# Kernel tuning notes

Measured on AMD Instinct MI355X. Metric: run time of the kernel, lower is better.

## Reference

```python
import jax, jax.numpy as jnp
import numpy as np

N, E, DIN, HID, G, L = 50000, 200000, 128, 128, 64, 6
H1, H2 = 8, 4
EPS_LN, EPS_BN = 1e-5, 1e-5


def setup_inputs() -> dict:
    key = jax.random.key(0)
    ks = iter(jax.random.split(key, 32))
    def nrm(shape, scale=0.05):
        return jax.random.normal(next(ks), shape, dtype=jnp.float32) * scale
    z = lambda *s: jnp.zeros(s, jnp.float32)
    o = lambda *s: jnp.ones(s, jnp.float32)
    return {
        'x': jax.random.normal(next(ks), (N, DIN), dtype=jnp.float32),
        'edge_index': jax.random.randint(next(ks), (2, E), 0, N),
        'batch': jnp.sort(jax.random.randint(next(ks), (N,), 0, G)),
        'W1': nrm((DIN, H1 * HID)), 'a_src1': nrm((H1, HID)), 'a_dst1': nrm((H1, HID)), 'b1': z(H1 * HID),
        'W2': nrm((H1 * HID, H2 * HID)), 'a_src2': nrm((H2, HID)), 'a_dst2': nrm((H2, HID)), 'b2': z(H2 * HID),
        'W3': nrm((H2 * HID, HID)), 'b3': z(HID),
        'wq': nrm((L, HID, HID)), 'bq': z(L, HID), 'wk': nrm((L, HID, HID)), 'bk': z(L, HID),
        'wv': nrm((L, HID, HID)), 'bv': z(L, HID), 'wo': nrm((L, HID, HID)), 'bo': z(L, HID),
        'ln1g': o(L, HID), 'ln1b': z(L, HID), 'ln2g': o(L, HID), 'ln2b': z(L, HID),
        'wf1': nrm((L, HID, 4 * HID)), 'bf1': z(L, 4 * HID), 'wf2': nrm((L, 4 * HID, HID)), 'bf2': z(L, HID),
        'bn1_g': o(2 * HID), 'bn1_b': z(2 * HID),
        'fc1_w': nrm((2 * HID, HID // 2)), 'fc1_b': z(HID // 2),
        'bn2_g': o(HID // 2), 'bn2_b': z(HID // 2),
        'fc2_w': nrm((HID // 2, 2)), 'fc2_b': z(2),
    }


def _ln(x, g, b):
    mu = x.mean(-1, keepdims=True)
    v = ((x - mu) ** 2).mean(-1, keepdims=True)
    return (x - mu) * jax.lax.rsqrt(v + EPS_LN) * g + b


def _gat(x, src, dst, W, a_s, a_d, b, heads):
    # PyG GATConv: message src -> dst, segment softmax over incoming edges per dst.
    h = (x @ W).reshape(x.shape[0], heads, -1)           # [N, H, C]
    e = jax.nn.leaky_relu((h * a_s).sum(-1)[src] + (h * a_d).sum(-1)[dst], 0.2)  # [E, H]
    m = jax.ops.segment_max(e, dst, num_segments=N)
    ex = jnp.exp(e - jnp.where(jnp.isfinite(m), m, 0.0)[dst])
    s = jax.ops.segment_sum(ex, dst, num_segments=N)
    alpha = ex / (s[dst] + 1e-16)
    out = jax.ops.segment_sum(alpha[:, :, None] * h[src], dst, num_segments=N)
    return out.reshape(N, -1) + b


def _forward(x, edge_index, batch, W1, a_src1, a_dst1, b1, W2, a_src2, a_dst2, b2, W3, b3,
             wq, bq, wk, bk, wv, bv, wo, bo, ln1g, ln1b, ln2g, ln2b, wf1, bf1, wf2, bf2,
             bn1_g, bn1_b, fc1_w, fc1_b, bn2_g, bn2_b, fc2_w, fc2_b):
    loop = jnp.arange(N, dtype=edge_index.dtype)
    src = jnp.concatenate([edge_index[0], loop])          # add self-loops (PyG default)
    dst = jnp.concatenate([edge_index[1], loop])
    h = jax.nn.elu(_gat(x, src, dst, W1, a_src1, a_dst1, b1, H1))
    h = jax.nn.elu(_gat(h, src, dst, W2, a_src2, a_dst2, b2, H2))
    # GCNConv with symmetric normalization (self-loops already included)
    deg = jax.ops.segment_sum(jnp.ones(src.shape, h.dtype), dst, num_segments=N)
    dinv = jnp.where(deg > 0, jax.lax.rsqrt(jnp.maximum(deg, 1e-12)), 0.0)
    norm = dinv[src] * dinv[dst]
    h = jax.nn.elu(jax.ops.segment_sum(norm[:, None] * (h @ W3)[src], dst, num_segments=N) + b3)
    # TransformerEncoder over seq_len=1 (h3.unsqueeze(1)): softmax over one key == 1,
    # so MHA output == Wo @ (Wv h + bv) + bo exactly; q/k have no effect on the output.
    for l in range(L):
        sa = (h @ wv[l] + bv[l]) @ wo[l] + bo[l]
        h = _ln(h + sa, ln1g[l], ln1b[l])
        ff = jax.nn.gelu(h @ wf1[l] + bf1[l], approximate=False) @ wf2[l] + bf2[l]
        h = _ln(h + ff, ln2g[l], ln2b[l])
    # global mean / max pool over graphs
    cnt = jax.ops.segment_sum(jnp.ones((N,), h.dtype), batch, num_segments=G)
    hm = jax.ops.segment_sum(h, batch, num_segments=G) / jnp.maximum(cnt, 1.0)[:, None]
    hx = jax.ops.segment_max(h, batch, num_segments=G)
    hx = jnp.where(jnp.isfinite(hx), hx, 0.0)
    hc = jnp.concatenate([hm, hx], axis=1)                # [G, 2*HID]
    bn_s = 1.0 / np.sqrt(1.0 + EPS_BN)                    # eval BN: running stats (0, 1)
    hc = hc * bn_s * bn1_g + bn1_b
    hc = jax.nn.elu(hc @ fc1_w + fc1_b)
    hc = hc * bn_s * bn2_g + bn2_b
    return hc @ fc2_w + fc2_b                             # [G, 2]


def reference(x, edge_index, batch, W1, a_src1, a_dst1, b1, W2, a_src2, a_dst2, b2, W3, b3,
              wq, bq, wk, bk, wv, bv, wo, bo, ln1g, ln1b, ln2g, ln2b, wf1, bf1, wf2, bf2,
              bn1_g, bn1_b, fc1_w, fc1_b, bn2_g, bn2_b, fc2_w, fc2_b):
    return _forward(x, edge_index, batch, W1, a_src1, a_dst1, b1, W2, a_src2, a_dst2, b2, W3, b3,
                    wq, bq, wk, bk, wv, bv, wo, bo, ln1g, ln1b, ln2g, ln2b, wf1, bf1, wf2, bf2,
                    bn1_g, bn1_b, fc1_w, fc1_b, bn2_g, bn2_b, fc2_w, fc2_b)
```

## Files before the change

kernel.cpp:

```cpp
#include <hip/hip_runtime.h>
#include <hip/hip_bf16.h>
#include <math.h>

#define NN 50000
#define EE 200000
#define ET 250000
#define GG 64
#define LL 6

using short8 = __attribute__((ext_vector_type(8))) short;
using f32x4  = __attribute__((ext_vector_type(4))) float;
typedef unsigned short ushortT;

__device__ __forceinline__ float elu1(float x) { return x > 0.f ? x : expm1f(x); }
__device__ __forceinline__ float gelu_exact(float x) {
    return 0.5f * x * (1.f + erff(x * 0.70710678118654752440f));
}
__device__ __forceinline__ short f2bf(float f) {
    __hip_bfloat16 h = __float2bfloat16(f);
    return *reinterpret_cast<short*>(&h);
}
__device__ __forceinline__ float bf2f(ushortT u) {
    return __uint_as_float(((unsigned)u) << 16);
}
__device__ __forceinline__ void accum8(float* acc, float a, uint4 d) {
    acc[0] += a * bf2f((ushortT)(d.x & 0xffff));
    acc[1] += a * bf2f((ushortT)(d.x >> 16));
    acc[2] += a * bf2f((ushortT)(d.y & 0xffff));
    acc[3] += a * bf2f((ushortT)(d.y >> 16));
    acc[4] += a * bf2f((ushortT)(d.z & 0xffff));
    acc[5] += a * bf2f((ushortT)(d.z >> 16));
    acc[6] += a * bf2f((ushortT)(d.w & 0xffff));
    acc[7] += a * bf2f((ushortT)(d.w >> 16));
}

__global__ void count_deg_kernel(const int* __restrict__ ei, int* __restrict__ deg) {
    int e = blockIdx.x * 256 + threadIdx.x;
    if (e >= ET) return;
    int dst = (e < EE) ? ei[EE + e] : (e - EE);
    atomicAdd(&deg[dst], 1);
}

__global__ void scan_kernel(const int* __restrict__ deg, int* __restrict__ row_ptr, int n) {
    __shared__ int s[1024];
    int tid = threadIdx.x;
    const int per = (n + 1023) / 1024;
    int lo = tid * per, hi = min(lo + per, n);
    int sum = 0;
    for (int i = lo; i < hi; i++) sum += deg[i];
    s[tid] = sum;
    __syncthreads();
    for (int off = 1; off < 1024; off <<= 1) {
        int t = (tid >= off) ? s[tid - off] : 0;
        __syncthreads();
        s[tid] += t;
        __syncthreads();
    }
    int run = s[tid] - sum;
    for (int i = lo; i < hi; i++) { row_ptr[i] = run; run += deg[i]; }
    if (tid == 1023) row_ptr[n] = s[1023];
}

__global__ void fill_csr_kernel(const int* __restrict__ ei, const int* __restrict__ row_ptr,
                                int* __restrict__ cursor, int* __restrict__ edge_src) {
    int e = blockIdx.x * 256 + threadIdx.x;
    if (e >= ET) return;
    int src, dst;
    if (e < EE) { src = ei[e]; dst = ei[EE + e]; }
    else        { src = e - EE; dst = e - EE; }
    int pos = atomicAdd(&cursor[dst], 1);
    edge_src[row_ptr[dst] + pos] = src;
}

__global__ void dinv_kernel(const int* __restrict__ row_ptr, float* __restrict__ dinv) {
    int n = blockIdx.x * 256 + threadIdx.x;
    if (n >= NN) return;
    int d = row_ptr[n + 1] - row_ptr[n];
    dinv[n] = (d > 0) ? rsqrtf((float)d) : 0.f;
}

__global__ void wvwo_kernel(const float* __restrict__ wv, const float* __restrict__ wo,
                            const float* __restrict__ bv, const float* __restrict__ bo,
                            float* __restrict__ Wvo, float* __restrict__ bvo) {
    int l = blockIdx.y;
    const float* Wv = wv + l * 16384;
    const float* Wo = wo + l * 16384;
    int tid = blockIdx.x * 256 + threadIdx.x;
    if (tid < 16384) {
        int r = tid >> 7, c = tid & 127;
        float s = 0.f;
        for (int k = 0; k < 128; k++) s += Wv[r * 128 + k] * Wo[k * 128 + c];
        Wvo[l * 16384 + tid] = s;
    }
    if (blockIdx.x == 0 && threadIdx.x < 128) {
        int c = threadIdx.x;
        float s = bo[l * 128 + c];
        for (int k = 0; k < 128; k++) s += bv[l * 128 + k] * Wo[k * 128 + c];
        bvo[l * 128 + c] = s;
    }
}

__global__ void bprep_kernel(const float* __restrict__ B, short* __restrict__ Bp,
                             int K, int N, int ldb, long srcStride) {
    int layer = blockIdx.y;
    const float* Bsrc = B + srcStride * layer;
    short* Bd = Bp + (size_t)K * N * layer;
    int total = (K >> 5) * (N >> 4) * 64;
    int tid = blockIdx.x * 256 + threadIdx.x;
    if (tid >= total) return;
    int l = tid & 63;
    int rest = tid >> 6;
    int kbc = K >> 5;
    int kb = rest % kbc;
    int c16 = rest / kbc;
    int n = c16 * 16 + (l & 15);
    int kbase = kb * 32 + (l >> 4) * 8;
    short v[8];
#pragma unroll
    for (int j = 0; j < 8; j++) v[j] = f2bf(Bsrc[(size_t)(kbase + j) * ldb + n]);
    *(uint4*)(Bd + (size_t)tid * 8) = *(uint4*)v;
}

__global__ void cast_bf16_kernel(const float* __restrict__ in, short* __restrict__ out, int n4) {
    int i = blockIdx.x * 256 + threadIdx.x;
    if (i >= n4) return;
    float4 v = *(const float4*)(in + (size_t)i * 4);
    short s[4] = { f2bf(v.x), f2bf(v.y), f2bf(v.z), f2bf(v.w) };
    *(uint2*)(out + (size_t)i * 4) = *(uint2*)s;
}

template <int EPI, bool BIAS, bool OUTBF16, int NSPLIT, int KBC,
          bool TMAJ = false, bool ATILE32 = false>
__global__ __launch_bounds__(256) void gemm_bf16_kernel(
    const short* __restrict__ A, const short* __restrict__ Bp,
    const float* __restrict__ bias, void* __restrict__ Cv,
    const float* __restrict__ a_s, const float* __restrict__ a_d,
    float* __restrict__ as_out, float* __restrict__ ad_out, int asH,
    const ushortT* __restrict__ Rres, const float* __restrict__ lng,
    const float* __restrict__ lnb, float* __restrict__ Qout,
    __hip_bfloat16* __restrict__ Qbout,
    int M, int K, int Nc) {
    __shared__ short Bs[(KBC > 0) ? KBC * 4096 : 8192];
    int t = threadIdx.x;
    int w = t >> 6, l = t & 63;
    int ln = l & 15, lq = l >> 4;
    int MBceil = (M + 63) >> 6;
    int bx = blockIdx.x;
    int xcd = bx & 7, idx = bx >> 3;
    int t2 = idx % NSPLIT;
    int mb = (idx / NSPLIT) * 8 + xcd;
    if (mb >= MBceil) return;
    int bm = mb * 64 + w * 16;
    int arow = bm + ln;
    bool aok = arow < M;
    int rowb = bm + lq * 4;
    const short* Ap = A + (size_t)arow * K + lq * 8;

    auto aload = [&](int kb) -> short8 {
        if (!aok) return (short8){0, 0, 0, 0, 0, 0, 0, 0};
        const short* p;
        if constexpr (ATILE32)
            p = A + ((size_t)kb * M + arow) * 32 + lq * 8;
        else
            p = Ap + kb * 32;
        return *(const short8*)p;
    };

    f32x4 acc[8];
#pragma unroll
    for (int j = 0; j < 8; j++) acc[j] = (f32x4){0.f, 0.f, 0.f, 0.f};

    if constexpr (KBC > 0) {
        {
            const uint4* src = (const uint4*)(Bp + (size_t)t2 * KBC * 4096);
            uint4* dst = (uint4*)Bs;
#pragma unroll
            for (int i = 0; i < KBC * 2; i++)
                dst[i * 256 + t] = src[i * 256 + t];
        }
        short8 af[KBC];
#pragma unroll
        for (int kb = 0; kb < KBC; kb++)
            af[kb] = aload(kb);
        __syncthreads();
#pragma unroll
        for (int kb = 0; kb < KBC; kb++)
#pragma unroll
            for (int ct = 0; ct < 8; ct++) {
                short8 bfr = *(const short8*)(Bs + ((ct * KBC + kb) * 64 + l) * 8);
                acc[ct] = __builtin_amdgcn_mfma_f32_16x16x32_bf16(af[kb], bfr, acc[ct], 0, 0, 0);
            }
    } else {
        int kbc = K >> 5;
        int sct = t >> 5, spart = t & 31;
        auto stage = [&](int buf, int kb) {
            const uint4* src = (const uint4*)(Bp + ((size_t)(t2 * 8 + sct) * kbc + kb) * 512);
            uint4* dst = (uint4*)(Bs + buf * 4096 + sct * 512);
            dst[spart * 2]     = src[spart * 2];
            dst[spart * 2 + 1] = src[spart * 2 + 1];
        };
        stage(0, 0);
        __syncthreads();
        for (int kb = 0; kb < kbc; kb++) {
            if (kb + 1 < kbc) stage((kb + 1) & 1, kb + 1);
            short8 af = aload(kb);
            const short* bsb = Bs + (kb & 1) * 4096;
#pragma unroll
            for (int ct = 0; ct < 8; ct++) {
                short8 bfr = *(const short8*)(bsb + (ct * 64 + l) * 8);
                acc[ct] = __builtin_amdgcn_mfma_f32_16x16x32_bf16(af, bfr, acc[ct], 0, 0, 0);
            }
            __syncthreads();
        }
    }

    if (EPI == 2) {
        const float* asv = a_s + t2 * 128;
        const float* adv = a_d + t2 * 128;
#pragma unroll
        for (int reg = 0; reg < 4; reg++) {
            float vs = 0.f, vd = 0.f;
#pragma unroll
            for (int ct = 0; ct < 8; ct++) {
                int colL = ct * 16 + ln;
                float av = acc[ct][reg];
                vs += av * asv[colL];
                vd += av * adv[colL];
            }
            vs += __shfl_xor(vs, 1); vs += __shfl_xor(vs, 2);
            vs += __shfl_xor(vs, 4); vs += __shfl_xor(vs, 8);
            vd += __shfl_xor(vd, 1); vd += __shfl_xor(vd, 2);
            vd += __shfl_xor(vd, 4); vd += __shfl_xor(vd, 8);
            int row = rowb + reg;
            if (ln == 0 && row < M) {
                as_out[(size_t)row * asH + t2] = vs;
                ad_out[(size_t)row * asH + t2] = vd;
            }
        }
    }
    if (EPI == 3) {
        float v[8][4];
#pragma unroll
        for (int ct = 0; ct < 8; ct++) {
            int col = ct * 16 + ln;
            float bv_ = bias[col];
#pragma unroll
            for (int reg = 0; reg < 4; reg++) {
                int row = rowb + reg;
                float r = (row < M) ? bf2f(Rres[(size_t)row * 128 + col]) : 0.f;
                v[ct][reg] = acc[ct][reg] + bv_ + r;
            }
        }
#pragma unroll
        for (int reg = 0; reg < 4; reg++) {
            float s = 0.f;
#pragma unroll
            for (int ct = 0; ct < 8; ct++) s += v[ct][reg];
            s += __shfl_xor(s, 1); s += __shfl_xor(s, 2);
            s += __shfl_xor(s, 4); s += __shfl_xor(s, 8);
            float mean = s * (1.f / 128.f);
            float s2 = 0.f;
#pragma unroll
            for (int ct = 0; ct < 8; ct++) { float d = v[ct][reg] - mean; s2 += d * d; }
            s2 += __shfl_xor(s2, 1); s2 += __shfl_xor(s2, 2);
            s2 += __shfl_xor(s2, 4); s2 += __shfl_xor(s2, 8);
            float rstd = rsqrtf(s2 * (1.f / 128.f) + 1e-5f);
            int row = rowb + reg;
            if (row < M) {
#pragma unroll
                for (int ct = 0; ct < 8; ct++) {
                    int col = ct * 16 + ln;
                    float o = (v[ct][reg] - mean) * rstd * lng[col] + lnb[col];
                    Qbout[(size_t)row * 128 + col] = __float2bfloat16(o);
                    if (Qout) Qout[(size_t)row * 128 + col] = o;
                }
            }
        }
    }
    if (EPI == 0 || EPI == 1 || EPI == 2) {
#pragma unroll
        for (int ct = 0; ct < 8; ct++) {
            int col = t2 * 128 + ct * 16 + ln;
            float bv_ = BIAS ? bias[col] : 0.f;
#pragma unroll
            for (int reg = 0; reg < 4; reg++) {
                int row = rowb + reg;
                if (row < M) {
                    float v = acc[ct][reg] + bv_;
                    if (EPI == 1) v = gelu_exact(v);
                    if (OUTBF16) {
                        size_t addr;
                        if constexpr (TMAJ)
                            addr = ((size_t)(col >> 5) * M + row) * 32 + (col & 31);
                        else
                            addr = (size_t)row * Nc + col;
                        ((__hip_bfloat16*)Cv)[addr] = __float2bfloat16(v);
                    } else {
                        ((float*)Cv)[(size_t)row * Nc + col] = v;
                    }
                }
            }
        }
    }
}

template <int H>
__global__ __launch_bounds__(256) void gat_alpha_kernel(
    const float* __restrict__ as_, const float* __restrict__ ad_,
    const int* __restrict__ row_ptr, const int* __restrict__ edge_src,
    float* __restrict__ exA, float* __restrict__ exS, int n_nodes) {
    const int GS = 64 / H;
    int node = blockIdx.x * 4 + (threadIdx.x >> 6);
    if (node >= n_nodes) return;
    int l = threadIdx.x & 63;
    int h = l / GS;
    int lig = l % GS;
    int start = row_ptr[node];
    int deg = row_ptr[node + 1] - start;
    float adn = ad_[(size_t)node * H + h];
    float m = -1e30f;
    for (int j = lig; j < deg; j += GS) {
        int s = edge_src[start + j];
        float e = as_[(size_t)s * H + h] + adn;
        e = e > 0.f ? e : 0.2f * e;
        m = fmaxf(m, e);
    }
#pragma unroll
    for (int mask = 1; mask < GS; mask <<= 1)
        m = fmaxf(m, __shfl_xor(m, mask));
    float S = 0.f;
    for (int j = lig; j < deg; j += GS) {
        int s = edge_src[start + j];
        float e = as_[(size_t)s * H + h] + adn;
        e = e > 0.f ? e : 0.2f * e;
        float ex = expf(e - m);
        exA[(size_t)h * ET + (start + j)] = ex;
        S += ex;
    }
#pragma unroll
    for (int mask = 1; mask < GS; mask <<= 1)
        S += __shfl_xor(S, mask);
    if (lig == 0) exS[(size_t)h * n_nodes + node] = S;
}

__global__ __launch_bounds__(256) void gat_agg_tiled_kernel(
    const ushortT* __restrict__ hT, const float* __restrict__ exA,
    const float* __restrict__ exS, const float* __restrict__ bias,
    const int* __restrict__ row_ptr, const int* __restrict__ edge_src,
    __hip_bfloat16* __restrict__ outT, int n_nodes, int NB) {
    int bx = blockIdx.x;
    int xcd = bx & 7, rest = bx >> 3;
    int tl = rest / NB, nb = rest - tl * NB;
    int tile = tl * 8 + xcd;
    int nl = threadIdx.x >> 2, q = threadIdx.x & 3;
    int node = nb * 64 + nl;
    if (node >= n_nodes) return;
    int hb = tile >> 2;
    const ushortT* __restrict__ base = hT + (size_t)tile * n_nodes * 32 + q * 8;
    const float* __restrict__ exAh = exA + (size_t)hb * ET;
    int start = row_ptr[node];
    int deg = row_ptr[node + 1] - start;
    float acc[8];
#pragma unroll
    for (int c = 0; c < 8; c++) acc[c] = 0.f;
    for (int j = 0; j < deg; j++) {
        int s = edge_src[start + j];
        float a = exAh[start + j];
        uint4 d = *(const uint4*)(base + (size_t)s * 32);
        accum8(acc, a, d);
    }
    float inv = 1.f / (exS[(size_t)hb * n_nodes + node] + 1e-16f);
    const float* bp = bias + tile * 32 + q * 8;
    short o[8];
#pragma unroll
    for (int c = 0; c < 8; c++)
        o[c] = f2bf(elu1(acc[c] * inv + bp[c]));
    *(uint4*)(outT + ((size_t)tile * n_nodes + node) * 32 + q * 8) = *(uint4*)o;
}

__global__ __launch_bounds__(256, 2) void gcn_agg_kernel(
    const ushortT* __restrict__ hp, const float* __restrict__ dinv,
    const float* __restrict__ b3, const int* __restrict__ row_ptr,
    const int* __restrict__ edge_src,
    __hip_bfloat16* __restrict__ outb, int n_nodes) {
    int node = blockIdx.x * 2 + (threadIdx.x >> 7);
    int c = threadIdx.x & 127;
    if (node >= n_nodes) return;
    int start = row_ptr[node];
    int deg = row_ptr[node + 1] - start;
    float dn = dinv[node];
    float acc = 0.f;
    auto LS = [&](int j) { return edge_src[start + min(j, deg - 1)]; };
    int s0 = LS(0), s1 = LS(1), s2 = LS(2), s3 = LS(3);
    int s4 = LS(4), s5 = LS(5), s6 = LS(6), s7 = LS(7);
    auto HW = [&](int s, int j, float& h, float& w) {
        h = bf2f(hp[(size_t)s * 128 + c]);
        w = (j < deg) ? dinv[s] * dn : 0.f;
    };
    float h0, h1, h2, h3, h4, h5, h6, h7;
    float w0, w1, w2, w3, w4, w5, w6, w7;
    HW(s0, 0, h0, w0); HW(s1, 1, h1, w1); HW(s2, 2, h2, w2); HW(s3, 3, h3, w3);
    HW(s4, 4, h4, w4); HW(s5, 5, h5, w5); HW(s6, 6, h6, w6); HW(s7, 7, h7, w7);
    int j0 = 0;
    while (true) {
        int jn = j0 + 8;
        bool more = jn < deg;
        float g0, g1, g2, g3, g4, g5, g6, g7;
        float v0 = 0.f, v1 = 0.f, v2 = 0.f, v3 = 0.f;
        float v4 = 0.f, v5 = 0.f, v6 = 0.f, v7 = 0.f;
        if (more) {
            int t0 = LS(jn),     t1 = LS(jn + 1), t2 = LS(jn + 2), t3 = LS(jn + 3);
            int t4 = LS(jn + 4), t5 = LS(jn + 5), t6 = LS(jn + 6), t7 = LS(jn + 7);
            HW(t0, jn,     g0, v0); HW(t1, jn + 1, g1, v1);
            HW(t2, jn + 2, g2, v2); HW(t3, jn + 3, g3, v3);
            HW(t4, jn + 4, g4, v4); HW(t5, jn + 5, g5, v5);
            HW(t6, jn + 6, g6, v6); HW(t7, jn + 7, g7, v7);
        }
        acc += w0 * h0 + w1 * h1 + w2 * h2 + w3 * h3
             + w4 * h4 + w5 * h5 + w6 * h6 + w7 * h7;
        if (!more) break;
        h0 = g0; h1 = g1; h2 = g2; h3 = g3;
        h4 = g4; h5 = g5; h6 = g6; h7 = g7;
        w0 = v0; w1 = v1; w2 = v2; w3 = v3;
        w4 = v4; w5 = v5; w6 = v6; w7 = v7;
        j0 = jn;
    }
    outb[(size_t)node * 128 + c] = __float2bfloat16(elu1(acc + b3[c]));
}

__global__ void pool1_kernel(const float* __restrict__ Q, const int* __restrict__ batch,
                             float* __restrict__ psum, float* __restrict__ pmax, int n_nodes) {
    int g = blockIdx.x, seg = blockIdx.y;
    int c = threadIdx.x;
    int lo, hi;
    {
        int l = 0, h = n_nodes;
        while (l < h) { int mid = (l + h) >> 1; if (batch[mid] < g) l = mid + 1; else h = mid; }
        lo = l;
        l = lo; h = n_nodes;
        while (l < h) { int mid = (l + h) >> 1; if (batch[mid] < g + 1) l = mid + 1; else h = mid; }
        hi = l;
    }
    int len = hi - lo;
    int a = lo + (int)((long)len * seg / 8);
    int b = lo + (int)((long)len * (seg + 1) / 8);
    float s = 0.f, mx = -INFINITY;
    for (int n = a; n < b; n++) {
        float v = Q[(size_t)n * 128 + c];
        s += v;
        mx = fmaxf(mx, v);
    }
    psum[(g * 8 + seg) * 128 + c] = s;
    pmax[(g * 8 + seg) * 128 + c] = mx;
}

__global__ void pool2_kernel(const float* __restrict__ psum, const float* __restrict__ pmax,
                             const int* __restrict__ batch,
                             const float* __restrict__ bn1g, const float* __restrict__ bn1b,
                             float* __restrict__ hc, int n_nodes) {
    int g = blockIdx.x;
    int c = threadIdx.x;
    int lo, hi;
    {
        int l = 0, h = n_nodes;
        while (l < h) { int mid = (l + h) >> 1; if (batch[mid] < g) l = mid + 1; else h = mid; }
        lo = l;
        l = lo; h = n_nodes;
        while (l < h) { int mid = (l + h) >> 1; if (batch[mid] < g + 1) l = mid + 1; else h = mid; }
        hi = l;
    }
    int cnt = hi - lo;
    float s = 0.f, mx = -INFINITY;
    for (int seg = 0; seg < 8; seg++) {
        s += psum[(g * 8 + seg) * 128 + c];
        mx = fmaxf(mx, pmax[(g * 8 + seg) * 128 + c]);
    }
    float hm = s / fmaxf((float)cnt, 1.f);
    float hx = (cnt > 0 && isfinite(mx)) ? mx : 0.f;
    const float bn_s = 0.99999500003749968f;
    hc[g * 256 + c]       = hm * bn_s * bn1g[c] + bn1b[c];
    hc[g * 256 + 128 + c] = hx * bn_s * bn1g[128 + c] + bn1b[128 + c];
}

__global__ void head_kernel(const float* __restrict__ hc,
                            const float* __restrict__ fc1w, const float* __restrict__ fc1b,
                            const float* __restrict__ bn2g, const float* __restrict__ bn2b,
                            const float* __restrict__ fc2w, const float* __restrict__ fc2b,
                            float* __restrict__ out) {
    int g = blockIdx.x;
    int j = threadIdx.x;
    const float bn_s = 0.99999500003749968f;
    float acc = fc1b[j];
    for (int i = 0; i < 256; i++) acc += hc[g * 256 + i] * fc1w[i * 64 + j];
    acc = elu1(acc);
    acc = acc * bn_s * bn2g[j] + bn2b[j];
    __shared__ float sv[64];
    sv[j] = acc;
    __syncthreads();
    if (j < 2) {
        float o = fc2b[j];
        for (int i = 0; i < 64; i++) o += sv[i] * fc2w[i * 2 + j];
        out[g * 2 + j] = o;
    }
}

extern "C" void kernel_launch(void* const* d_in, const int* in_sizes, int n_in,
                              void* d_out, int out_size, void* d_ws, size_t ws_size,
                              hipStream_t stream) {
    const float* x    = (const float*)d_in[0];
    const int*   ei   = (const int*)d_in[1];
    const int*   batch= (const int*)d_in[2];
    const float* W1   = (const float*)d_in[3];
    const float* as1  = (const float*)d_in[4];
    const float* ad1  = (const float*)d_in[5];
    const float* b1   = (const float*)d_in[6];
    const float* W2   = (const float*)d_in[7];
    const float* as2  = (const float*)d_in[8];
    const float* ad2  = (const float*)d_in[9];
    const float* b2   = (const float*)d_in[10];
    const float* W3   = (const float*)d_in[11];
    const float* b3   = (const float*)d_in[12];
    const float* wv   = (const float*)d_in[17];
    const float* bv   = (const float*)d_in[18];
    const float* wo   = (const float*)d_in[19];
    const float* bo   = (const float*)d_in[20];
    const float* ln1g = (const float*)d_in[21];
    const float* ln1b = (const float*)d_in[22];
    const float* ln2g = (const float*)d_in[23];
    const float* ln2b = (const float*)d_in[24];
    const float* wf1  = (const float*)d_in[25];
    const float* bf1  = (const float*)d_in[26];
    const float* wf2  = (const float*)d_in[27];
    const float* bf2  = (const float*)d_in[28];
    const float* bn1g = (const float*)d_in[29];
    const float* bn1b = (const float*)d_in[30];
    const float* fc1w = (const float*)d_in[31];
    const float* fc1b = (const float*)d_in[32];
    const float* bn2g = (const float*)d_in[33];
    const float* bn2b = (const float*)d_in[34];
    const float* fc2w = (const float*)d_in[35];
    const float* fc2b = (const float*)d_in[36];
    float* out = (float*)d_out;

    char* wsb = (char*)d_ws;
    short* xb    = (short*)wsb;
    float* exAf  = (float*)wsb;
    float* exSf  = (float*)(wsb + 8000000);
    short* h1t   = (short*)(wsb + 12800000);
    short* h2t   = (short*)(wsb + 12800000);
    short* h3pre = (short*)(wsb + 12800000);
    short* FFb   = (short*)(wsb + 25600000);
    short* bh1   = (short*)(wsb + 115200000);
    short* bh2   = (short*)(wsb + 115200000);
    float* fQ    = (float*)(wsb + 128000000);
    short* Qb    = (short*)(wsb + 153600000);
    char* tail = wsb + 217600000;
    short* W1p  = (short*)tail;  tail += 262144;
    short* W2p  = (short*)tail;  tail += 1048576;
    short* W3p  = (short*)tail;  tail += 131072;
    short* Wvop = (short*)tail;  tail += 196608;
    short* wf1p = (short*)tail;  tail += 786432;
    short* wf2p = (short*)tail;  tail += 786432;
    float* Wvo  = (float*)tail;  tail += 393216;
    float* bvo  = (float*)tail;  tail += 3072;
    float* fAS  = (float*)tail;  tail += 1600000;
    float* fAD  = (float*)tail;  tail += 1600000;
    float* fDv  = (float*)tail;  tail += 200000;
    float* psum = (float*)tail;  tail += 262144;
    float* pmax = (float*)tail;  tail += 262144;
    float* fHC  = (float*)tail;  tail += 65536;
    int* iDeg   = (int*)tail;    tail += 200000;
    int* iRP    = (int*)tail;    tail += 200004;
    int* iCur   = (int*)tail;    tail += 200000;
    int* iES    = (int*)tail;    tail += 1000000;

    hipMemsetAsync(iDeg, 0, NN * sizeof(int), stream);
    hipMemsetAsync(iCur, 0, NN * sizeof(int), stream);

    count_deg_kernel<<<(ET + 255) / 256, 256, 0, stream>>>(ei, iDeg);
    scan_kernel<<<1, 1024, 0, stream>>>(iDeg, iRP, NN);
    fill_csr_kernel<<<(ET + 255) / 256, 256, 0, stream>>>(ei, iRP, iCur, iES);
    dinv_kernel<<<(NN + 255) / 256, 256, 0, stream>>>(iRP, fDv);

    wvwo_kernel<<<dim3(64, 6), 256, 0, stream>>>(wv, wo, bv, bo, Wvo, bvo);
    auto bprep = [&](const float* B, short* Bp, int K, int N, int ldb, long sStride, int layers) {
        int total = (K >> 5) * (N >> 4) * 64;
        dim3 grid((total + 255) / 256, layers);
        bprep_kernel<<<grid, 256, 0, stream>>>(B, Bp, K, N, ldb, sStride);
    };
    bprep(W1, W1p, 128, 1024, 1024, 0, 1);
    bprep(W2, W2p, 1024, 512, 512, 0, 1);
    bprep(W3, W3p, 512, 128, 128, 0, 1);
    bprep(Wvo, Wvop, 128, 128, 128, 16384, 6);
    bprep(wf1, wf1p, 128, 512, 512, 65536, 6);
    bprep(wf2, wf2p, 512, 128, 128, 65536, 6);
    cast_bf16_kernel<<<(NN * 128 / 4 + 255) / 256, 256, 0, stream>>>(x, xb, NN * 128 / 4);

    const int MB64 = (NN + 63) / 64;
    const int MBp = ((MB64 + 7) / 8) * 8;
    const int NB = (NN + 63) / 64;

    gemm_bf16_kernel<2, false, true, 8, 4, true, false><<<MBp * 8, 256, 0, stream>>>(
        xb, W1p, nullptr, h1t, as1, ad1, fAS, fAD, 8,
        nullptr, nullptr, nullptr, nullptr, nullptr, NN, 128, 1024);
    gat_alpha_kernel<8><<<(NN + 3) / 4, 256, 0, stream>>>(
        fAS, fAD, iRP, iES, exAf, exSf, NN);
    gat_agg_tiled_kernel<<<4 * NB * 8, 256, 0, stream>>>(
        (const ushortT*)h1t, exAf, exSf, b1, iRP, iES, (__hip_bfloat16*)bh1, NN, NB);
    gemm_bf16_kernel<2, false, true, 4, 0, true, true><<<MBp * 4, 256, 0, stream>>>(
        bh1, W2p, nullptr, h2t, as2, ad2, fAS, fAD, 4,
        nullptr, nullptr, nullptr, nullptr, nullptr, NN, 1024, 512);
    gat_alpha_kernel<4><<<(NN + 3) / 4, 256, 0, stream>>>(
        fAS, fAD, iRP, iES, exAf, exSf, NN);
    gat_agg_tiled_kernel<<<2 * NB * 8, 256, 0, stream>>>(
        (const ushortT*)h2t, exAf, exSf, b2, iRP, iES, (__hip_bfloat16*)bh2, NN, NB);
    gemm_bf16_kernel<0, false, true, 1, 0, false, true><<<MBp, 256, 0, stream>>>(
        bh2, W3p, nullptr, h3pre, nullptr, nullptr, nullptr, nullptr, 0,
        nullptr, nullptr, nullptr, nullptr, nullptr, NN, 512, 128);
    gcn_agg_kernel<<<(NN + 1) / 2, 256, 0, stream>>>(
        (const ushortT*)h3pre, fDv, b3, iRP, iES, (__hip_bfloat16*)Qb, NN);
    for (int l = 0; l < LL; l++) {
        gemm_bf16_kernel<3, true, false, 1, 4><<<MBp, 256, 0, stream>>>(
            Qb, Wvop + l * 16384, bvo + l * 128, nullptr, nullptr, nullptr, nullptr, nullptr, 0,
            (const ushortT*)Qb, ln1g + l * 128, ln1b + l * 128, nullptr, (__hip_bfloat16*)Qb,
            NN, 128, 128);
        gemm_bf16_kernel<1, true, true, 4, 4><<<MBp * 4, 256, 0, stream>>>(
            Qb, wf1p + l * 65536, bf1 + l * 512, FFb, nullptr, nullptr, nullptr, nullptr, 0,
            nullptr, nullptr, nullptr, nullptr, nullptr, NN, 128, 512);
        gemm_bf16_kernel<3, true, false, 1, 0><<<MBp, 256, 0, stream>>>(
            FFb, wf2p + l * 65536, bf2 + l * 128, nullptr, nullptr, nullptr, nullptr, nullptr, 0,
            (const ushortT*)Qb, ln2g + l * 128, ln2b + l * 128,
            (l == LL - 1) ? fQ : nullptr, (__hip_bfloat16*)Qb, NN, 512, 128);
    }
    pool1_kernel<<<dim3(GG, 8), 128, 0, stream>>>(fQ, batch, psum, pmax, NN);
    pool2_kernel<<<GG, 128, 0, stream>>>(psum, pmax, batch, bn1g, bn1b, fHC, NN);
    head_kernel<<<GG, 64, 0, stream>>>(fHC, fc1w, fc1b, bn2g, bn2b, fc2w, fc2b, out);
}
```

Measured before the change: 1.308 ms.

## Sort nodes by degree before GAT aggregation to balance wavefront work

Adds a counting sort of nodes by in-degree (histogram, 64-bucket scan, scatter) that builds a permutation. The GAT aggregation kernels then process nodes in permuted order, so lanes in a wavefront have similar edge-loop trip counts and diverge less. The cost is three small extra kernels plus an indirect node lookup. Output writes and exS reads become scattered, which loses the coalescing of the original node order.

Result: slower. 1.768 ms (+35.2%).

```diff
diff --git a/kernel.cpp b/kernel.cpp
--- a/kernel.cpp
+++ b/kernel.cpp
@@ -77,6 +77,33 @@
     if (n >= NN) return;
     int d = row_ptr[n + 1] - row_ptr[n];
     dinv[n] = (d > 0) ? rsqrtf((float)d) : 0.f;
+}
+
+__global__ void hist_deg_kernel(const int* __restrict__ row_ptr, int* __restrict__ hist) {
+    int n = blockIdx.x * 256 + threadIdx.x;
+    if (n >= NN) return;
+    int d = min(row_ptr[n + 1] - row_ptr[n], 63);
+    atomicAdd(&hist[d], 1);
+}
+__global__ void scan64_kernel(int* __restrict__ hist) {
+    __shared__ int s[64];
+    int t = threadIdx.x;
+    s[t] = hist[t];
+    __syncthreads();
+    if (t == 0) {
+        int run = 0;
+        for (int i = 0; i < 64; i++) { int v = s[i]; s[i] = run; run += v; }
+    }
+    __syncthreads();
+    hist[t] = s[t];
+}
+__global__ void scatter_perm_kernel(const int* __restrict__ row_ptr,
+                                    int* __restrict__ hist, int* __restrict__ perm) {
+    int n = blockIdx.x * 256 + threadIdx.x;
+    if (n >= NN) return;
+    int d = min(row_ptr[n + 1] - row_ptr[n], 63);
+    int p = atomicAdd(&hist[d], 1);
+    perm[p] = n;
 }
 
 __global__ void wvwo_kernel(const float* __restrict__ wv, const float* __restrict__ wo,
@@ -347,14 +374,16 @@
     const ushortT* __restrict__ hT, const float* __restrict__ exA,
     const float* __restrict__ exS, const float* __restrict__ bias,
     const int* __restrict__ row_ptr, const int* __restrict__ edge_src,
+    const int* __restrict__ perm,
     __hip_bfloat16* __restrict__ outT, int n_nodes, int NB) {
     int bx = blockIdx.x;
     int xcd = bx & 7, rest = bx >> 3;
     int tl = rest / NB, nb = rest - tl * NB;
     int tile = tl * 8 + xcd;
     int nl = threadIdx.x >> 2, q = threadIdx.x & 3;
-    int node = nb * 64 + nl;
-    if (node >= n_nodes) return;
+    int idx = nb * 64 + nl;
+    if (idx >= n_nodes) return;
+    int node = perm[idx];
     int hb = tile >> 2;
     const ushortT* __restrict__ base = hT + (size_t)tile * n_nodes * 32 + q * 8;
     const float* __restrict__ exAh = exA + (size_t)hb * ET;
@@ -581,6 +610,11 @@
     scan_kernel<<<1, 1024, 0, stream>>>(iDeg, iRP, NN);
     fill_csr_kernel<<<(ET + 255) / 256, 256, 0, stream>>>(ei, iRP, iCur, iES);
     dinv_kernel<<<(NN + 255) / 256, 256, 0, stream>>>(iRP, fDv);
+    int* perm = iCur;
+    hipMemsetAsync(iDeg, 0, 64 * sizeof(int), stream);
+    hist_deg_kernel<<<(NN + 255) / 256, 256, 0, stream>>>(iRP, iDeg);
+    scan64_kernel<<<1, 64, 0, stream>>>(iDeg);
+    scatter_perm_kernel<<<(NN + 255) / 256, 256, 0, stream>>>(iRP, iDeg, perm);
 
     wvwo_kernel<<<dim3(64, 6), 256, 0, stream>>>(wv, wo, bv, bo, Wvo, bvo);
     auto bprep = [&](const float* B, short* Bp, int K, int N, int ldb, long sStride, int layers) {
@@ -606,14 +640,14 @@
     gat_alpha_kernel<8><<<(NN + 3) / 4, 256, 0, stream>>>(
         fAS, fAD, iRP, iES, exAf, exSf, NN);
     gat_agg_tiled_kernel<<<4 * NB * 8, 256, 0, stream>>>(
-        (const ushortT*)h1t, exAf, exSf, b1, iRP, iES, (__hip_bfloat16*)bh1, NN, NB);
+        (const ushortT*)h1t, exAf, exSf, b1, iRP, iES, perm, (__hip_bfloat16*)bh1, NN, NB);
     gemm_bf16_kernel<2, false, true, 4, 0, true, true><<<MBp * 4, 256, 0, stream>>>(
         bh1, W2p, nullptr, h2t, as2, ad2, fAS, fAD, 4,
         nullptr, nullptr, nullptr, nullptr, nullptr, NN, 1024, 512);
     gat_alpha_kernel<4><<<(NN + 3) / 4, 256, 0, stream>>>(
         fAS, fAD, iRP, iES, exAf, exSf, NN);
     gat_agg_tiled_kernel<<<2 * NB * 8, 256, 0, stream>>>(
-        (const ushortT*)h2t, exAf, exSf, b2, iRP, iES, (__hip_bfloat16*)bh2, NN, NB);
+        (const ushortT*)h2t, exAf, exSf, b2, iRP, iES, perm, (__hip_bfloat16*)bh2, NN, NB);
     gemm_bf16_kernel<0, false, true, 1, 0, false, true><<<MBp, 256, 0, stream>>>(
         bh2, W3p, nullptr, h3pre, nullptr, nullptr, nullptr, nullptr, 0,
         nullptr, nullptr, nullptr, nullptr, nullptr, NN, 512, 128);
```
